# Kernel optimization log

Hardware: AMD Instinct MI355X
Metric: run time of the kernel (lower is better)

The kernel has to match this reference:

```python
import jax, jax.numpy as jnp
import numpy as np

NA, NB_N, ND = 100000, 100000, 50000   # nodes per ntype a, b, d
H, OUT = 128, 16                        # hidden dim, num classes
NUM_BASES, NREL, E = 2, 4, 600000       # basis decomposition, relations, edges/rel
RELS = [('a', 'd'), ('b', 'd'), ('d', 'a'), ('d', 'b')]  # sorted rel canonical types
NT = {'a': NA, 'b': NB_N, 'd': ND}


def setup_inputs() -> dict:
    key = jax.random.key(0)
    ks = jax.random.split(key, 32)
    inp = {
        'feat_a': jax.random.normal(ks[0], (NA, H), jnp.float32),
        'feat_b': jax.random.normal(ks[1], (NB_N, H), jnp.float32),
        'feat_d': jax.random.normal(ks[2], (ND, H), jnp.float32),
    }
    # 3 layers: h->h, h->h, h->out; basis-decomposed relation weights + layer bias
    for l, (din, dout) in enumerate([(H, H), (H, H), (H, OUT)]):
        inp[f'basis{l}'] = jax.random.normal(ks[3 + 3 * l], (NUM_BASES, din, dout), jnp.float32) / np.sqrt(din)
        inp[f'coef{l}'] = jax.random.normal(ks[4 + 3 * l], (NREL, NUM_BASES), jnp.float32)
        inp[f'bias{l}'] = jnp.zeros((dout,), jnp.float32)
    # edge lists per relation (src indexes src-ntype, dst indexes dst-ntype)
    for r, (st, dt) in enumerate(RELS):
        inp[f'e{r}_src'] = jax.random.randint(ks[16 + 2 * r], (E,), 0, NT[st], jnp.int32)
        inp[f'e{r}_dst'] = jax.random.randint(ks[17 + 2 * r], (E,), 0, NT[dt], jnp.int32)
    return inp


def _rel_layer(h, basis, coef, bias, edges, act):
    # W_r = sum_b coef[r,b] * basis[b]  -> [NREL, din, dout]
    W = jnp.einsum('rb,bio->rio', coef, basis)
    dout = W.shape[-1]
    out = {nt: jnp.zeros((n, dout), W.dtype) for nt, n in NT.items()}
    for r, (st, dt) in enumerate(RELS):
        src, dst = edges[r]
        # aggregate-then-transform (linear commutes with the sum): saves FLOPs+memory
        agg = jax.ops.segment_sum(h[st][src], dst, num_segments=NT[dt])  # [Ndt, din]
        deg = jax.ops.segment_sum(jnp.ones((src.shape[0],), W.dtype), dst, num_segments=NT[dt])
        agg = agg / jnp.maximum(deg, 1.0)[:, None]  # norm='right' (in-degree, clamp 1)
        out[dt] = out[dt] + agg @ W[r]
    if act:
        return {k: jax.nn.relu(v + bias) for k, v in out.items()}
    return {k: v + bias for k, v in out.items()}


def reference(feat_a, feat_b, feat_d,
              basis0, coef0, bias0, basis1, coef1, bias1, basis2, coef2, bias2,
              e0_src, e0_dst, e1_src, e1_dst, e2_src, e2_dst, e3_src, e3_dst):
    edges = [(e0_src, e0_dst), (e1_src, e1_dst), (e2_src, e2_dst), (e3_src, e3_dst)]
    h = {'a': feat_a, 'b': feat_b, 'd': feat_d}
    h = _rel_layer(h, basis0, coef0, bias0, edges, True)
    h = _rel_layer(h, basis1, coef1, bias1, edges, True)
    h = _rel_layer(h, basis2, coef2, bias2, edges, False)
    return h['d']  # eval-mode output of EntityClassify
```

## Files before the change

### kernel.cpp

```cpp
#include <hip/hip_runtime.h>

#define NA 100000
#define NB 100000
#define ND 50000
#define HDIM 128
#define DOUT 16
#define NODE_TOT (2*ND + NA + NB)
#define BSH 9
#define BKN 512
#define NBUCKET ((NODE_TOT + BKN - 1) >> BSH)
#define BCAP 8192
#define EPB 4096
#define TP 136

typedef __attribute__((ext_vector_type(8))) short short8v;
typedef __attribute__((ext_vector_type(4))) float f32x4;

__device__ __forceinline__ unsigned short f2bf(float f) {
    unsigned u = __float_as_uint(f);
    return (unsigned short)((u + 0x7fffu + ((u >> 16) & 1u)) >> 16);
}
__device__ __forceinline__ void addbf2(float& x, float& y, unsigned u) {
    x += __uint_as_float(u << 16);
    y += __uint_as_float(u & 0xffff0000u);
}

__device__ __forceinline__ void gather_row(const unsigned int* __restrict__ tbl,
                                           const int* __restrict__ csr,
                                           int s0, int deg, int q,
                                           float& a0, float& a1, float& a2, float& a3,
                                           float& a4, float& a5, float& a6, float& a7) {
    for (int j = 0; j < deg; j += 16) {
        int cnt = deg - j; if (cnt > 16) cnt = 16;
        int myidx = (j + q < deg) ? csr[s0 + j + q] : 0;
        uint4 v[8];
        #pragma unroll
        for (int k = 0; k < 8; ++k)
            v[k] = *(const uint4*)(tbl + (size_t)__shfl(myidx, k, 16)*64 + q*4);
        #pragma unroll
        for (int k = 0; k < 8; ++k)
            if (k < cnt) { addbf2(a0,a1,v[k].x); addbf2(a2,a3,v[k].y);
                           addbf2(a4,a5,v[k].z); addbf2(a6,a7,v[k].w); }
        if (cnt > 8) {
            #pragma unroll
            for (int k = 8; k < 16; ++k)
                v[k-8] = *(const uint4*)(tbl + (size_t)__shfl(myidx, k, 16)*64 + q*4);
            #pragma unroll
            for (int k = 8; k < 16; ++k)
                if (k < cnt) { addbf2(a0,a1,v[k-8].x); addbf2(a2,a3,v[k-8].y);
                               addbf2(a4,a5,v[k-8].z); addbf2(a6,a7,v[k-8].w); }
        }
    }
}

struct EdgeT { int node; int src; };
__device__ __forceinline__ EdgeT edge_at(int g,
    const int* __restrict__ s0, const int* __restrict__ d0,
    const int* __restrict__ s1, const int* __restrict__ d1,
    const int* __restrict__ s2, const int* __restrict__ d2,
    const int* __restrict__ s3, const int* __restrict__ d3,
    int E0, int E1, int E2) {
    EdgeT e;
    if (g < E0)             { e.node = d0[g];                    e.src = s0[g]; }
    else if (g < E0+E1)     { e.node = ND + d1[g-E0];            e.src = s1[g-E0]; }
    else if (g < E0+E1+E2)  { e.node = 2*ND + d2[g-E0-E1];       e.src = s2[g-E0-E1]; }
    else                    { e.node = 2*ND+NA + d3[g-E0-E1-E2]; e.src = s3[g-E0-E1-E2]; }
    return e;
}

__global__ __launch_bounds__(256) void k_weights(const float* __restrict__ basis,
                                                 const float* __restrict__ coef,
                                                 float* __restrict__ W0, float* __restrict__ W1,
                                                 int r0, int r1, int n) {
    int i = blockIdx.x * 256 + threadIdx.x;
    if (i >= n) return;
    float b0 = basis[i], b1 = basis[n + i];
    W0[i] = coef[r0*2+0]*b0 + coef[r0*2+1]*b1;
    W1[i] = coef[r1*2+0]*b0 + coef[r1*2+1]*b1;
}

__global__ __launch_bounds__(256) void k_weights_bfT(const float* __restrict__ basis,
                                                     const float* __restrict__ coef,
                                                     unsigned short* __restrict__ WT0,
                                                     unsigned short* __restrict__ WT1,
                                                     int r0, int r1) {
    int i = blockIdx.x * 256 + threadIdx.x;
    if (i >= HDIM*HDIM) return;
    int k = i >> 7, j = i & 127;
    float b0 = basis[i], b1 = basis[HDIM*HDIM + i];
    WT0[(size_t)j*HDIM + k] = f2bf(coef[r0*2+0]*b0 + coef[r0*2+1]*b1);
    WT1[(size_t)j*HDIM + k] = f2bf(coef[r1*2+0]*b0 + coef[r1*2+1]*b1);
}

__global__ __launch_bounds__(256) void k_cvt_bf16_ab(const float* __restrict__ ina,
                                                     const float* __restrict__ inb,
                                                     unsigned int* __restrict__ outa,
                                                     unsigned int* __restrict__ outb) {
    int i = blockIdx.x * 256 + threadIdx.x;
    const float* in; unsigned int* out;
    if (i < NA*16) { in = ina; out = outa; }
    else           { in = inb; out = outb; i -= NA*16; }
    const float4 a = *(const float4*)(in + (size_t)i*8);
    const float4 b = *(const float4*)(in + (size_t)i*8 + 4);
    uint4 p;
    p.x = (unsigned)f2bf(a.x) | ((unsigned)f2bf(a.y) << 16);
    p.y = (unsigned)f2bf(a.z) | ((unsigned)f2bf(a.w) << 16);
    p.z = (unsigned)f2bf(b.x) | ((unsigned)f2bf(b.y) << 16);
    p.w = (unsigned)f2bf(b.z) | ((unsigned)f2bf(b.w) << 16);
    *(uint4*)(out + (size_t)i*4) = p;
}

__global__ __launch_bounds__(256) void k_ginit(int* __restrict__ gcur) {
    int i = blockIdx.x * 256 + threadIdx.x;
    if (i < NBUCKET) gcur[i] = i * BCAP;
}

__global__ __launch_bounds__(256) void k_bscatter(const int* __restrict__ s0, const int* __restrict__ d0,
                                                  const int* __restrict__ s1, const int* __restrict__ d1,
                                                  const int* __restrict__ s2, const int* __restrict__ d2,
                                                  const int* __restrict__ s3, const int* __restrict__ d3,
                                                  int E0, int E1, int E2, int Etot,
                                                  int* __restrict__ gcur,
                                                  unsigned int* __restrict__ pairs) {
    __shared__ int hist[NBUCKET];
    __shared__ int base[NBUCKET];
    for (int i = threadIdx.x; i < NBUCKET; i += 256) hist[i] = 0;
    __syncthreads();
    int g0 = blockIdx.x * EPB + threadIdx.x;
    int nd[EPB/256], sr[EPB/256], rk[EPB/256];
    #pragma unroll
    for (int i = 0; i < EPB/256; ++i) {
        int g = g0 + i*256;
        if (g < Etot) {
            EdgeT e = edge_at(g, s0,d0,s1,d1,s2,d2,s3,d3, E0,E1,E2);
            nd[i] = e.node; sr[i] = e.src;
            rk[i] = atomicAdd(&hist[e.node >> BSH], 1);
        } else nd[i] = -1;
    }
    __syncthreads();
    for (int i = threadIdx.x; i < NBUCKET; i += 256)
        if (hist[i]) base[i] = atomicAdd(&gcur[i], hist[i]);
    __syncthreads();
    #pragma unroll
    for (int i = 0; i < EPB/256; ++i) {
        if (nd[i] >= 0) {
            unsigned p = ((unsigned)(nd[i] & (BKN-1)) << 17) | (unsigned)sr[i];
            pairs[base[nd[i] >> BSH] + rk[i]] = p;
        }
    }
}

__global__ __launch_bounds__(256) void k_bdeg(const unsigned int* __restrict__ pairs,
                                              const int* __restrict__ gcur,
                                              int* __restrict__ deg) {
    __shared__ int ld[BKN];
    int b = blockIdx.x;
    for (int i = threadIdx.x; i < BKN; i += 256) ld[i] = 0;
    __syncthreads();
    int j0 = b * BCAP, j1 = gcur[b];
    for (int j = j0 + threadIdx.x; j < j1; j += 256)
        atomicAdd(&ld[pairs[j] >> 17], 1);
    __syncthreads();
    int nbase = b << BSH;
    for (int i = threadIdx.x; i < BKN && nbase + i < NODE_TOT; i += 256)
        deg[nbase + i] = ld[i];
}

__global__ __launch_bounds__(256) void k_bfill(const unsigned int* __restrict__ pairs,
                                               const int* __restrict__ gcur,
                                               const int* __restrict__ offs,
                                               int* __restrict__ csr) {
    __shared__ int cur[BKN];
    int b = blockIdx.x;
    int nbase = b << BSH;
    for (int i = threadIdx.x; i < BKN && nbase + i < NODE_TOT; i += 256)
        cur[i] = offs[nbase + i];
    __syncthreads();
    int j0 = b * BCAP, j1 = gcur[b];
    for (int j = j0 + threadIdx.x; j < j1; j += 256) {
        unsigned e = pairs[j];
        int p = atomicAdd(&cur[e >> 17], 1);
        csr[p] = (int)(e & 0x1FFFFu);
    }
}

__global__ __launch_bounds__(1024) void k_scan1(const int* __restrict__ deg,
                                                int* __restrict__ offs,
                                                int* __restrict__ bsum, int N) {
    __shared__ int sh[1024];
    int i = blockIdx.x * 1024 + threadIdx.x;
    int v = (i < N) ? deg[i] : 0;
    sh[threadIdx.x] = v;
    __syncthreads();
    for (int off = 1; off < 1024; off <<= 1) {
        int t = (threadIdx.x >= off) ? sh[threadIdx.x - off] : 0;
        __syncthreads();
        sh[threadIdx.x] += t;
        __syncthreads();
    }
    if (i < N) offs[i + 1] = sh[threadIdx.x];
    if (threadIdx.x == 1023) bsum[blockIdx.x] = sh[1023];
    if (i == 0) offs[0] = 0;
}

__global__ __launch_bounds__(1024) void k_scan2(int* __restrict__ bsum, int nb) {
    __shared__ int sh[1024];
    int t = threadIdx.x;
    sh[t] = (t < nb) ? bsum[t] : 0;
    __syncthreads();
    for (int off = 1; off < 1024; off <<= 1) {
        int v = (t >= off) ? sh[t - off] : 0;
        __syncthreads();
        sh[t] += v;
        __syncthreads();
    }
    if (t < nb) bsum[t] = sh[t];
}

__global__ __launch_bounds__(1024) void k_scan3(int* __restrict__ offs,
                                                const int* __restrict__ bsum, int N) {
    int i = blockIdx.x * 1024 + threadIdx.x;
    if (blockIdx.x > 0 && i < N) offs[i + 1] += bsum[blockIdx.x - 1];
}

__global__ __launch_bounds__(256) void k_gfused_l01(const unsigned int* __restrict__ fa,
                                                    const unsigned int* __restrict__ fb,
                                                    const int* __restrict__ offs,
                                                    const int* __restrict__ csr,
                                                    const unsigned short* __restrict__ WT0,
                                                    const unsigned short* __restrict__ WT1,
                                                    const unsigned short* __restrict__ WT12,
                                                    const unsigned short* __restrict__ WT13,
                                                    const float* __restrict__ bias,
                                                    unsigned short* __restrict__ t2out,
                                                    unsigned short* __restrict__ t3out,
                                                    int nrows) {
    __shared__ unsigned short tA[16 * TP];
    __shared__ unsigned short tB[16 * TP];
    const int t = threadIdx.x;
    const int row0 = blockIdx.x * 16;
    const int l = t & 63, wid = t >> 6;
    const int colw = wid * 32;
    const int rl = l & 15, kq = l >> 4, kl = kq * 8;
    const int q = t & 15, gslot = t >> 4;

    #pragma unroll
    for (int h = 0; h < 2; ++h) {
        const unsigned int* tbl = h ? fb : fa;
        unsigned short* tile = h ? tB : tA;
        const int row = row0 + gslot;
        float a0=0,a1=0,a2=0,a3=0,a4=0,a5=0,a6=0,a7=0;
        int deg = 0;
        if (row < nrows) {
            int node = (h ? ND : 0) + row;
            int s0 = offs[node];
            deg = offs[node + 1] - s0;
            gather_row(tbl, csr, s0, deg, q, a0,a1,a2,a3,a4,a5,a6,a7);
        }
        float sc = 1.0f / fmaxf((float)deg, 1.0f);
        uint4 o;
        o.x = (unsigned)f2bf(a0*sc) | ((unsigned)f2bf(a1*sc) << 16);
        o.y = (unsigned)f2bf(a2*sc) | ((unsigned)f2bf(a3*sc) << 16);
        o.z = (unsigned)f2bf(a4*sc) | ((unsigned)f2bf(a5*sc) << 16);
        o.w = (unsigned)f2bf(a6*sc) | ((unsigned)f2bf(a7*sc) << 16);
        *(uint4*)(tile + gslot*TP + q*8) = o;
    }
    __syncthreads();

    f32x4 acc[2];
    acc[0] = (f32x4)0.f; acc[1] = (f32x4)0.f;
    #pragma unroll
    for (int h = 0; h < 2; ++h) {
        const unsigned short* tile = h ? tB : tA;
        const unsigned short* WT = h ? WT1 : WT0;
        #pragma unroll
        for (int s = 0; s < 4; ++s) {
            const int k0 = s * 32;
            short8v a = *(const short8v*)(tile + rl*TP + k0 + kl);
            #pragma unroll
            for (int cf = 0; cf < 2; ++cf) {
                short8v b = *(const short8v*)(WT + (size_t)(colw + cf*16 + rl)*HDIM + k0 + kl);
                acc[cf] = __builtin_amdgcn_mfma_f32_16x16x32_bf16(a, b, acc[cf], 0, 0, 0);
            }
        }
    }
    __syncthreads();

    #pragma unroll
    for (int cf = 0; cf < 2; ++cf) {
        const float bc = bias[colw + cf*16 + rl];
        #pragma unroll
        for (int j = 0; j < 4; ++j)
            tA[(kq*4 + j)*TP + colw + cf*16 + rl] = f2bf(fmaxf(acc[cf][j] + bc, 0.f));
    }
    __syncthreads();

    #pragma unroll
    for (int h2 = 0; h2 < 2; ++h2) {
        const unsigned short* WT = h2 ? WT13 : WT12;
        unsigned short* outp = h2 ? t3out : t2out;
        f32x4 a2[2];
        a2[0] = (f32x4)0.f; a2[1] = (f32x4)0.f;
        #pragma unroll
        for (int s = 0; s < 4; ++s) {
            const int k0 = s * 32;
            short8v a = *(const short8v*)(tA + rl*TP + k0 + kl);
            #pragma unroll
            for (int cf = 0; cf < 2; ++cf) {
                short8v b = *(const short8v*)(WT + (size_t)(colw + cf*16 + rl)*HDIM + k0 + kl);
                a2[cf] = __builtin_amdgcn_mfma_f32_16x16x32_bf16(a, b, a2[cf], 0, 0, 0);
            }
        }
        #pragma unroll
        for (int cf = 0; cf < 2; ++cf)
            #pragma unroll
            for (int j = 0; j < 4; ++j) {
                int row = row0 + kq*4 + j;
                if (row < nrows)
                    outp[(size_t)row*HDIM + colw + cf*16 + rl] = f2bf(a2[cf][j]);
            }
    }
}

__global__ __launch_bounds__(256) void k_gather_trans16_ab(const unsigned int* __restrict__ t2,
                                                           const unsigned int* __restrict__ t3,
                                                           const int* __restrict__ offs,
                                                           const int* __restrict__ csr,
                                                           const float* __restrict__ bias,
                                                           const float* __restrict__ W20,
                                                           const float* __restrict__ W21,
                                                           float* __restrict__ t1a,
                                                           float* __restrict__ t1b) {
    __shared__ float WlT[16 * 132];
    __shared__ float vbuf[16 * 132];
    const int t = threadIdx.x;
    const bool blkA = (blockIdx.x < NA/16);
    const float* W = blkA ? W20 : W21;
    {
        const int jj = t & 15, c0 = (t >> 4) * 8;
        #pragma unroll
        for (int i = 0; i < 8; ++i)
            WlT[jj*132 + c0 + i] = W[(size_t)(c0 + i)*DOUT + jj];
    }
    __syncthreads();
    const int w = t >> 6, l = t & 63;
    const int sub = l >> 4, q = l & 15;
    const int lrow = w * 4 + sub;
    const int node = 2*ND + blockIdx.x * 16 + lrow;
    const unsigned int* tbl = blkA ? t2 : t3;
    const int s0 = offs[node];
    const int deg = offs[node + 1] - s0;
    float a0=0,a1=0,a2=0,a3=0,a4=0,a5=0,a6=0,a7=0;
    gather_row(tbl, csr, s0, deg, q, a0,a1,a2,a3,a4,a5,a6,a7);
    const float sc = 1.0f / fmaxf((float)deg, 1.0f);
    const float4 bi0 = *(const float4*)(bias + q*8);
    const float4 bi1 = *(const float4*)(bias + q*8 + 4);
    float4 v0, v1;
    v0.x = fmaxf(a0*sc + bi0.x, 0.f); v0.y = fmaxf(a1*sc + bi0.y, 0.f);
    v0.z = fmaxf(a2*sc + bi0.z, 0.f); v0.w = fmaxf(a3*sc + bi0.w, 0.f);
    v1.x = fmaxf(a4*sc + bi1.x, 0.f); v1.y = fmaxf(a5*sc + bi1.y, 0.f);
    v1.z = fmaxf(a6*sc + bi1.z, 0.f); v1.w = fmaxf(a7*sc + bi1.w, 0.f);
    *(float4*)(vbuf + lrow*132 + q*8)     = v0;
    *(float4*)(vbuf + lrow*132 + q*8 + 4) = v1;
    __syncthreads();
    const int rr = t >> 4, jj = t & 15;
    const float* vr = vbuf + rr*132;
    const float* wr = WlT + jj*132;
    float4 acc4 = make_float4(0.f, 0.f, 0.f, 0.f);
    #pragma unroll 8
    for (int c4 = 0; c4 < 32; ++c4) {
        const float4 v = *(const float4*)(vr + c4*4);
        const float4 ww = *(const float4*)(wr + c4*4);
        acc4.x += v.x*ww.x; acc4.y += v.y*ww.y; acc4.z += v.z*ww.z; acc4.w += v.w*ww.w;
    }
    float acc = (acc4.x + acc4.y) + (acc4.z + acc4.w);
    const int grow = blockIdx.x * 16 + rr;
    if (blkA) t1a[(size_t)grow*DOUT + jj] = acc;
    else      t1b[(size_t)(grow - NA)*DOUT + jj] = acc;
}

__global__ __launch_bounds__(256) void k_gather16_combine(const float* __restrict__ t0,
                                                          const float* __restrict__ t1,
                                                          const int* __restrict__ offs0,
                                                          const int* __restrict__ offs1,
                                                          const int* __restrict__ csr,
                                                          const float* __restrict__ bias,
                                                          float* __restrict__ out, int nrows) {
    int t = threadIdx.x;
    int row = blockIdx.x * 64 + (t >> 2);
    if (row >= nrows) return;
    int q = t & 3;
    int c = q * 4;
    float4 acc = make_float4(0.f, 0.f, 0.f, 0.f);
    {
        int s0 = offs0[row], deg = offs0[row + 1] - s0;
        for (int j = 0; j < deg; j += 4) {
            int cnt = deg - j; if (cnt > 4) cnt = 4;
            int myidx = (j + q < deg) ? csr[s0 + j + q] : 0;
            float4 v[4];
            #pragma unroll
            for (int k = 0; k < 4; ++k)
                v[k] = *reinterpret_cast<const float4*>(t0 + (size_t)__shfl(myidx, k, 4)*DOUT + c);
            #pragma unroll
            for (int k = 0; k < 4; ++k)
                if (k < cnt) { acc.x += v[k].x; acc.y += v[k].y; acc.z += v[k].z; acc.w += v[k].w; }
        }
        float sc = 1.0f / fmaxf((float)deg, 1.0f);
        acc.x *= sc; acc.y *= sc; acc.z *= sc; acc.w *= sc;
    }
    float4 acc2 = make_float4(0.f, 0.f, 0.f, 0.f);
    {
        int u0 = offs1[row], deg = offs1[row + 1] - u0;
        for (int j = 0; j < deg; j += 4) {
            int cnt = deg - j; if (cnt > 4) cnt = 4;
            int myidx = (j + q < deg) ? csr[u0 + j + q] : 0;
            float4 v[4];
            #pragma unroll
            for (int k = 0; k < 4; ++k)
                v[k] = *reinterpret_cast<const float4*>(t1 + (size_t)__shfl(myidx, k, 4)*DOUT + c);
            #pragma unroll
            for (int k = 0; k < 4; ++k)
                if (k < cnt) { acc2.x += v[k].x; acc2.y += v[k].y; acc2.z += v[k].z; acc2.w += v[k].w; }
        }
        float sc2 = 1.0f / fmaxf((float)deg, 1.0f);
        acc2.x *= sc2; acc2.y *= sc2; acc2.z *= sc2; acc2.w *= sc2;
    }
    float4 bi = *reinterpret_cast<const float4*>(bias + c);
    acc.x += acc2.x + bi.x; acc.y += acc2.y + bi.y;
    acc.z += acc2.z + bi.z; acc.w += acc2.w + bi.w;
    *reinterpret_cast<float4*>(out + (size_t)row*DOUT + c) = acc;
}

extern "C" void kernel_launch(void* const* d_in, const int* in_sizes, int n_in,
                              void* d_out, int out_size, void* d_ws, size_t ws_size,
                              hipStream_t stream) {
    const float* feat_a = (const float*)d_in[0];
    const float* feat_b = (const float*)d_in[1];
    const float* basis0 = (const float*)d_in[3];
    const float* coef0  = (const float*)d_in[4];
    const float* bias0  = (const float*)d_in[5];
    const float* basis1 = (const float*)d_in[6];
    const float* coef1  = (const float*)d_in[7];
    const float* bias1  = (const float*)d_in[8];
    const float* basis2 = (const float*)d_in[9];
    const float* coef2  = (const float*)d_in[10];
    const float* bias2  = (const float*)d_in[11];
    const int* s0 = (const int*)d_in[12]; const int* d0 = (const int*)d_in[13];
    const int* s1 = (const int*)d_in[14]; const int* d1 = (const int*)d_in[15];
    const int* s2 = (const int*)d_in[16]; const int* d2 = (const int*)d_in[17];
    const int* s3 = (const int*)d_in[18]; const int* d3 = (const int*)d_in[19];
    const int E0 = in_sizes[12], E1 = in_sizes[14], E2 = in_sizes[16], E3 = in_sizes[18];
    const int Etot = E0 + E1 + E2 + E3;

    char* base = (char*)d_ws;
    auto alloc = [&](size_t bytes) { char* p = base; base += (bytes + 255) & ~(size_t)255; return p; };
    unsigned short* WT00 = (unsigned short*)alloc(HDIM*HDIM*2);
    unsigned short* WT01 = (unsigned short*)alloc(HDIM*HDIM*2);
    unsigned short* WT12 = (unsigned short*)alloc(HDIM*HDIM*2);
    unsigned short* WT13 = (unsigned short*)alloc(HDIM*HDIM*2);
    float* W20 = (float*)alloc(HDIM*DOUT*4);
    float* W21 = (float*)alloc(HDIM*DOUT*4);
    int* offs_all = (int*)alloc((NODE_TOT + 1) * 4);
    int* csr_all  = (int*)alloc((size_t)Etot * 4);
    int* bsum     = (int*)alloc(2048 * 4);
    int* deg      = (int*)alloc(NODE_TOT * 4);
    int* gcur     = (int*)alloc(NBUCKET * 4);
    unsigned int* pairs = (unsigned int*)alloc((size_t)NBUCKET * BCAP * 4);
    unsigned int* fa_bf  = (unsigned int*)alloc((size_t)NA*HDIM*2);
    unsigned int* fb_bf  = (unsigned int*)alloc((size_t)NB*HDIM*2);
    unsigned int* t2_bf  = (unsigned int*)alloc((size_t)ND*HDIM*2);
    unsigned int* t3_bf  = (unsigned int*)alloc((size_t)ND*HDIM*2);
    float* t1a  = (float*)alloc((size_t)NA*DOUT*4);
    float* t1b  = (float*)alloc((size_t)NB*DOUT*4);
    float* out = (float*)d_out;

    const int* offsR[2] = {offs_all, offs_all + ND};
    const int nbE = (Etot + EPB - 1) / EPB;

    k_weights_bfT<<<(HDIM*HDIM+255)/256, 256, 0, stream>>>(basis0, coef0, WT00, WT01, 0, 1);
    k_weights_bfT<<<(HDIM*HDIM+255)/256, 256, 0, stream>>>(basis1, coef1, WT12, WT13, 2, 3);
    k_weights<<<(HDIM*DOUT+255)/256, 256, 0, stream>>>(basis2, coef2, W20, W21, 0, 1, HDIM*DOUT);
    k_cvt_bf16_ab<<<((NA+NB)*16)/256, 256, 0, stream>>>(feat_a, feat_b, fa_bf, fb_bf);

    {
        k_ginit<<<(NBUCKET+255)/256, 256, 0, stream>>>(gcur);
        k_bscatter<<<nbE, 256, 0, stream>>>(s0,d0,s1,d1,s2,d2,s3,d3, E0,E1,E2, Etot, gcur, pairs);
        k_bdeg<<<NBUCKET, 256, 0, stream>>>(pairs, gcur, deg);
        int nb = (NODE_TOT + 1023) / 1024;
        k_scan1<<<nb, 1024, 0, stream>>>(deg, offs_all, bsum, NODE_TOT);
        k_scan2<<<1, 1024, 0, stream>>>(bsum, nb);
        k_scan3<<<nb, 1024, 0, stream>>>(offs_all, bsum, NODE_TOT);
        k_bfill<<<NBUCKET, 256, 0, stream>>>(pairs, gcur, offs_all, csr_all);
    }

    k_gfused_l01<<<(ND+15)/16, 256, 0, stream>>>(fa_bf, fb_bf, offs_all, csr_all,
                                                 WT00, WT01, WT12, WT13, bias0,
                                                 (unsigned short*)t2_bf, (unsigned short*)t3_bf, ND);

    k_gather_trans16_ab<<<(NA+NB)/16, 256, 0, stream>>>(t2_bf, t3_bf, offs_all, csr_all,
                                                        bias1, W20, W21, t1a, t1b);

    k_gather16_combine<<<(ND+63)/64, 256, 0, stream>>>(t1a, t1b, offsR[0], offsR[1], csr_all,
                                                       bias2, out, ND);
}
```

Before: 241.8 us.

## Fuse CSR degree count, scan and fill into one per-bucket kernel

Replaces the five-kernel CSR build (bucket degree count, three-stage global scan over node degrees, bucket fill) with a single scan over bucket counts plus one per-bucket kernel. That kernel loads the bucket's pairs into shared memory, counts degrees, does a local scan to write offsets, and fills the CSR. The aim is to cut launches and avoid reading the pairs array from global memory twice. Separately, the gather loop now loads the next chunk's neighbour indices at the end of each iteration, a small software prefetch. The 32KB of shared memory per block may limit occupancy.

```diff
diff --git a/kernel.cpp b/kernel.cpp
--- a/kernel.cpp
+++ b/kernel.cpp
@@ -30,9 +30,9 @@
                                            int s0, int deg, int q,
                                            float& a0, float& a1, float& a2, float& a3,
                                            float& a4, float& a5, float& a6, float& a7) {
+    int myidx = (q < deg) ? csr[s0 + q] : 0;
     for (int j = 0; j < deg; j += 16) {
         int cnt = deg - j; if (cnt > 16) cnt = 16;
-        int myidx = (j + q < deg) ? csr[s0 + j + q] : 0;
         uint4 v[8];
         #pragma unroll
         for (int k = 0; k < 8; ++k)
@@ -50,6 +50,7 @@
                 if (k < cnt) { addbf2(a0,a1,v[k-8].x); addbf2(a2,a3,v[k-8].y);
                                addbf2(a4,a5,v[k-8].z); addbf2(a6,a7,v[k-8].w); }
         }
+        myidx = (j + 16 + q < deg) ? csr[s0 + j + 16 + q] : 0;
     }
 }
 
@@ -150,63 +151,12 @@
     }
 }
 
-__global__ __launch_bounds__(256) void k_bdeg(const unsigned int* __restrict__ pairs,
-                                              const int* __restrict__ gcur,
-                                              int* __restrict__ deg) {
-    __shared__ int ld[BKN];
-    int b = blockIdx.x;
-    for (int i = threadIdx.x; i < BKN; i += 256) ld[i] = 0;
-    __syncthreads();
-    int j0 = b * BCAP, j1 = gcur[b];
-    for (int j = j0 + threadIdx.x; j < j1; j += 256)
-        atomicAdd(&ld[pairs[j] >> 17], 1);
-    __syncthreads();
-    int nbase = b << BSH;
-    for (int i = threadIdx.x; i < BKN && nbase + i < NODE_TOT; i += 256)
-        deg[nbase + i] = ld[i];
-}
-
-__global__ __launch_bounds__(256) void k_bfill(const unsigned int* __restrict__ pairs,
-                                               const int* __restrict__ gcur,
-                                               const int* __restrict__ offs,
-                                               int* __restrict__ csr) {
-    __shared__ int cur[BKN];
-    int b = blockIdx.x;
-    int nbase = b << BSH;
-    for (int i = threadIdx.x; i < BKN && nbase + i < NODE_TOT; i += 256)
-        cur[i] = offs[nbase + i];
-    __syncthreads();
-    int j0 = b * BCAP, j1 = gcur[b];
-    for (int j = j0 + threadIdx.x; j < j1; j += 256) {
-        unsigned e = pairs[j];
-        int p = atomicAdd(&cur[e >> 17], 1);
-        csr[p] = (int)(e & 0x1FFFFu);
-    }
-}
-
-__global__ __launch_bounds__(1024) void k_scan1(const int* __restrict__ deg,
-                                                int* __restrict__ offs,
-                                                int* __restrict__ bsum, int N) {
-    __shared__ int sh[1024];
-    int i = blockIdx.x * 1024 + threadIdx.x;
-    int v = (i < N) ? deg[i] : 0;
-    sh[threadIdx.x] = v;
-    __syncthreads();
-    for (int off = 1; off < 1024; off <<= 1) {
-        int t = (threadIdx.x >= off) ? sh[threadIdx.x - off] : 0;
-        __syncthreads();
-        sh[threadIdx.x] += t;
-        __syncthreads();
-    }
-    if (i < N) offs[i + 1] = sh[threadIdx.x];
-    if (threadIdx.x == 1023) bsum[blockIdx.x] = sh[1023];
-    if (i == 0) offs[0] = 0;
-}
-
-__global__ __launch_bounds__(1024) void k_scan2(int* __restrict__ bsum, int nb) {
+__global__ __launch_bounds__(1024) void k_bucket_scan(const int* __restrict__ gcur,
+                                                      int* __restrict__ cbase) {
     __shared__ int sh[1024];
     int t = threadIdx.x;
-    sh[t] = (t < nb) ? bsum[t] : 0;
+    int cntv = (t < NBUCKET) ? (gcur[t] - t * BCAP) : 0;
+    sh[t] = cntv;
     __syncthreads();
     for (int off = 1; off < 1024; off <<= 1) {
         int v = (t >= off) ? sh[t - off] : 0;
@@ -214,13 +164,48 @@
         sh[t] += v;
         __syncthreads();
     }
-    if (t < nb) bsum[t] = sh[t];
-}
-
-__global__ __launch_bounds__(1024) void k_scan3(int* __restrict__ offs,
-                                                const int* __restrict__ bsum, int N) {
-    int i = blockIdx.x * 1024 + threadIdx.x;
-    if (blockIdx.x > 0 && i < N) offs[i + 1] += bsum[blockIdx.x - 1];
+    if (t < NBUCKET) cbase[t] = sh[t] - cntv;
+}
+
+__global__ __launch_bounds__(256) void k_bfinal(const unsigned int* __restrict__ pairs,
+                                                const int* __restrict__ gcur,
+                                                const int* __restrict__ cbase,
+                                                int* __restrict__ offs,
+                                                int* __restrict__ csr, int Etot) {
+    __shared__ unsigned lp[BCAP];
+    __shared__ int ldeg[BKN];
+    __shared__ int lcur[BKN];
+    __shared__ int part[256];
+    const int t = threadIdx.x;
+    const int b = blockIdx.x;
+    const int cnt = gcur[b] - b * BCAP;
+    const int cb = cbase[b];
+    for (int i = t; i < cnt; i += 256) lp[i] = pairs[(size_t)b * BCAP + i];
+    for (int i = t; i < BKN; i += 256) ldeg[i] = 0;
+    __syncthreads();
+    for (int i = t; i < cnt; i += 256) atomicAdd(&ldeg[lp[i] >> 17], 1);
+    __syncthreads();
+    const int d0 = ldeg[2*t], d1 = ldeg[2*t + 1];
+    part[t] = d0 + d1;
+    __syncthreads();
+    for (int off = 1; off < 256; off <<= 1) {
+        int v = (t >= off) ? part[t - off] : 0;
+        __syncthreads();
+        part[t] += v;
+        __syncthreads();
+    }
+    const int excl = t ? part[t - 1] : 0;
+    const int nbase = b << BSH;
+    const int n0 = nbase + 2*t, n1 = n0 + 1;
+    if (n0 < NODE_TOT) { offs[n0] = cb + excl;      lcur[2*t]     = cb + excl; }
+    if (n1 < NODE_TOT) { offs[n1] = cb + excl + d0; lcur[2*t + 1] = cb + excl + d0; }
+    if (b == NBUCKET - 1 && t == 0) offs[NODE_TOT] = Etot;
+    __syncthreads();
+    for (int i = t; i < cnt; i += 256) {
+        unsigned e = lp[i];
+        int p = atomicAdd(&lcur[e >> 17], 1);
+        csr[p] = (int)(e & 0x1FFFFu);
+    }
 }
 
 __global__ __launch_bounds__(256) void k_gfused_l01(const unsigned int* __restrict__ fa,
@@ -462,9 +447,8 @@
     float* W21 = (float*)alloc(HDIM*DOUT*4);
     int* offs_all = (int*)alloc((NODE_TOT + 1) * 4);
     int* csr_all  = (int*)alloc((size_t)Etot * 4);
-    int* bsum     = (int*)alloc(2048 * 4);
-    int* deg      = (int*)alloc(NODE_TOT * 4);
     int* gcur     = (int*)alloc(NBUCKET * 4);
+    int* cbase    = (int*)alloc(NBUCKET * 4);
     unsigned int* pairs = (unsigned int*)alloc((size_t)NBUCKET * BCAP * 4);
     unsigned int* fa_bf  = (unsigned int*)alloc((size_t)NA*HDIM*2);
     unsigned int* fb_bf  = (unsigned int*)alloc((size_t)NB*HDIM*2);
@@ -485,12 +469,8 @@
     {
         k_ginit<<<(NBUCKET+255)/256, 256, 0, stream>>>(gcur);
         k_bscatter<<<nbE, 256, 0, stream>>>(s0,d0,s1,d1,s2,d2,s3,d3, E0,E1,E2, Etot, gcur, pairs);
-        k_bdeg<<<NBUCKET, 256, 0, stream>>>(pairs, gcur, deg);
-        int nb = (NODE_TOT + 1023) / 1024;
-        k_scan1<<<nb, 1024, 0, stream>>>(deg, offs_all, bsum, NODE_TOT);
-        k_scan2<<<1, 1024, 0, stream>>>(bsum, nb);
-        k_scan3<<<nb, 1024, 0, stream>>>(offs_all, bsum, NODE_TOT);
-        k_bfill<<<NBUCKET, 256, 0, stream>>>(pairs, gcur, offs_all, csr_all);
+        k_bucket_scan<<<1, 1024, 0, stream>>>(gcur, cbase);
+        k_bfinal<<<NBUCKET, 256, 0, stream>>>(pairs, gcur, cbase, offs_all, csr_all, Etot);
     }
 
     k_gfused_l01<<<(ND+15)/16, 256, 0, stream>>>(fa_bf, fb_bf, offs_all, csr_all,
```

New measurement: 229.3 us. -5.2%, faster.
